# Performance work log

Measured on AMD Instinct MI355X. Metric: run time of the kernel, lower is better.

The kernel has to match this reference:

```python
import jax, jax.numpy as jnp
import numpy as np

N_NODES = 100000
N_EDGES = 1600000
NODE_DIM = 128
HIDDEN_DIM = 128


def _sage_conv(x, src, dst, deg_inv, W_l, W_r, b):
    # PyG SAGEConv (aggr='mean', root_weight=True):
    #   out = lin_l(mean_{j in N(i)} x_j) + lin_r(x_i)
    msgs = x[src]                                             # [E, d_in] gather
    agg = jax.ops.segment_sum(msgs, dst, num_segments=N_NODES)  # [N, d_in]
    mean = agg * deg_inv[:, None]
    return mean @ W_l + x @ W_r + b


def setup_inputs() -> dict:
    key = jax.random.key(0)
    ks = jax.random.split(key, 9)
    x = jax.random.normal(ks[0], (N_NODES, NODE_DIM), dtype=jnp.float32)
    edge_index = jax.random.randint(ks[1], (2, N_EDGES), 0, N_NODES, dtype=jnp.int32)
    t = jnp.zeros((1,), dtype=jnp.float32)

    def glorot(k, fan_in, fan_out):
        s = (6.0 / (fan_in + fan_out)) ** 0.5
        return jax.random.uniform(k, (fan_in, fan_out), jnp.float32, -s, s)

    return {
        "t": t,
        "x": x,
        "edge_index": edge_index,
        "W1_l": glorot(ks[2], NODE_DIM, HIDDEN_DIM),
        "W1_r": glorot(ks[3], NODE_DIM, HIDDEN_DIM),
        "b1": jnp.zeros((HIDDEN_DIM,), jnp.float32),
        "W2_l": glorot(ks[4], HIDDEN_DIM, HIDDEN_DIM),
        "W2_r": glorot(ks[5], HIDDEN_DIM, HIDDEN_DIM),
        "b2": jnp.zeros((HIDDEN_DIM,), jnp.float32),
        "W3_l": glorot(ks[6], HIDDEN_DIM, NODE_DIM),
        "W3_r": glorot(ks[7], HIDDEN_DIM, NODE_DIM),
        "b3": jnp.zeros((NODE_DIM,), jnp.float32),
    }


def reference(t, x, edge_index, W1_l, W1_r, b1, W2_l, W2_r, b2, W3_l, W3_r, b3):
    src, dst = edge_index[0], edge_index[1]
    deg = jax.ops.segment_sum(jnp.ones((N_EDGES,), x.dtype), dst, num_segments=N_NODES)
    deg_inv = jnp.where(deg > 0, 1.0 / jnp.maximum(deg, 1.0), 0.0)

    h = jax.nn.relu(_sage_conv(x, src, dst, deg_inv, W1_l, W1_r, b1))
    h = jax.nn.relu(_sage_conv(h, src, dst, deg_inv, W2_l, W2_r, b2))
    dx_dt = _sage_conv(h, src, dst, deg_inv, W3_l, W3_r, b3)
    return dx_dt
```

## Files before the change

### kernel.cpp

```cpp
#include <hip/hip_runtime.h>

#define NN   100000
#define NE   1600000
#define DIM  128
#define NBKT 391
#define EPB  16384
#define NBLK 98
#define NTILES (NN / 16)
#define CASTB 12500
#define CWB   384

#define NSLC 8
#define GCH  512
#define GATB (((NN + GCH - 1) / GCH) * NSLC)

typedef short          s16x8 __attribute__((ext_vector_type(8)));
typedef unsigned short u16x8 __attribute__((ext_vector_type(8)));
typedef float          f32x4 __attribute__((ext_vector_type(4)));

__device__ __forceinline__ unsigned short f2b(float f) {
    unsigned u = __float_as_uint(f);
    unsigned r = ((u >> 16) & 1u) + 0x7FFFu;
    return (unsigned short)((u + r) >> 16);
}
__device__ __forceinline__ float b2f(unsigned short h) {
    return __uint_as_float(((unsigned)h) << 16);
}

__global__ void k_prep(const float* __restrict__ x, unsigned short* __restrict__ xb,
                       const int* __restrict__ dst, int* __restrict__ hist,
                       const float* __restrict__ W1l, const float* __restrict__ W1r,
                       const float* __restrict__ W2l, const float* __restrict__ W2r,
                       const float* __restrict__ W3l, const float* __restrict__ W3r,
                       unsigned short* __restrict__ Wt1, unsigned short* __restrict__ Wt2,
                       unsigned short* __restrict__ Wt3) {
    __shared__ int lh[NBKT];
    int t = threadIdx.x, b = blockIdx.x;
    if (b < NBLK) {
        for (int j = t; j < NBKT; j += 256) lh[j] = 0;
        __syncthreads();
        int base = b * EPB;
        int end = base + EPB; if (end > NE) end = NE;
        for (int i = base + t; i < end; i += 256) atomicAdd(&lh[dst[i] >> 8], 1);
        __syncthreads();
        for (int j = t; j < NBKT; j += 256) hist[j * NBLK + b] = lh[j];
    } else if (b < NBLK + CASTB) {
        int i = (b - NBLK) * 256 + t;
        int slice = i / (NN * 4);
        int rem = i - slice * (NN * 4);
        int node = rem >> 2;
        int off4 = i & 3;
        float4 v = ((const float4*)x)[node * 32 + slice * 4 + off4];
        ushort4 o;
        o.x = f2b(v.x); o.y = f2b(v.y); o.z = f2b(v.z); o.w = f2b(v.w);
        ((ushort4*)xb)[i] = o;
    } else {
        int i = (b - NBLK - CASTB) * 256 + t;
        int L = i >> 15;
        int rem = i & 32767;
        int n = rem >> 8;
        int k = rem & 255;
        const float* Wl = (L == 0) ? W1l : (L == 1) ? W2l : W3l;
        const float* Wr = (L == 0) ? W1r : (L == 1) ? W2r : W3r;
        unsigned short* Wt = (L == 0) ? Wt1 : (L == 1) ? Wt2 : Wt3;
        float v = (k < 128) ? Wl[k * 128 + n] : Wr[(k - 128) * 128 + n];
        Wt[n * 256 + k] = f2b(v);
    }
}

__global__ void k_scanrow(int* __restrict__ hist, int* __restrict__ row_total) {
    __shared__ int sh[128];
    int k = blockIdx.x, t = threadIdx.x;
    int v = (t < NBLK) ? hist[k * NBLK + t] : 0;
    sh[t] = v;
    __syncthreads();
    for (int off = 1; off < 128; off <<= 1) {
        int a = (t >= off) ? sh[t - off] : 0;
        __syncthreads();
        sh[t] += a;
        __syncthreads();
    }
    if (t < NBLK) hist[k * NBLK + t] = sh[t] - v;
    if (t == 127) row_total[k] = sh[127];
}

__global__ void k_scanbkt(const int* __restrict__ row_total, int* __restrict__ bbase) {
    __shared__ int sh[512];
    int t = threadIdx.x;
    int v = (t < NBKT) ? row_total[t] : 0;
    sh[t] = v;
    __syncthreads();
    for (int off = 1; off < 512; off <<= 1) {
        int a = (t >= off) ? sh[t - off] : 0;
        __syncthreads();
        sh[t] += a;
        __syncthreads();
    }
    if (t < NBKT) bbase[t] = sh[t] - v;
    if (t == NBKT) bbase[NBKT] = NE;
}

__global__ void k_bin2(const int* __restrict__ src, const int* __restrict__ dst,
                       const int* __restrict__ hist, const int* __restrict__ bbase,
                       int* __restrict__ binned) {
    __shared__ int s_base[NBKT];
    __shared__ int s_cnt[NBKT];
    int t = threadIdx.x, b = blockIdx.x;
    for (int j = t; j < NBKT; j += 256) {
        s_base[j] = bbase[j] + hist[j * NBLK + b];
        s_cnt[j] = 0;
    }
    __syncthreads();
    int base = b * EPB;
    int end = base + EPB; if (end > NE) end = NE;
    for (int i = base + t; i < end; i += 256) {
        int d = dst[i];
        int k = d >> 8;
        int w = (src[i] << 8) | (d & 255);
        int lpos = atomicAdd(&s_cnt[k], 1);
        binned[s_base[k] + lpos] = w;
    }
}

__global__ void k_build(const int* __restrict__ binned,
                        const int* __restrict__ bucket_base,
                        int* __restrict__ csr,
                        int* __restrict__ row_start,
                        float* __restrict__ deg_inv) {
    __shared__ int s_deg[256], s_scan[256], s_cur[256];
    __shared__ int stage[8192];
    int b = blockIdx.x, t = threadIdx.x;
    int base = bucket_base[b], end = bucket_base[b + 1];
    int cnt = end - base;
    s_deg[t] = 0;
    __syncthreads();
    for (int i = t; i < cnt; i += 256)
        atomicAdd(&s_deg[binned[base + i] & 255], 1);
    __syncthreads();
    s_scan[t] = s_deg[t];
    __syncthreads();
    for (int off = 1; off < 256; off <<= 1) {
        int a = (t >= off) ? s_scan[t - off] : 0;
        __syncthreads();
        s_scan[t] += a;
        __syncthreads();
    }
    int excl = s_scan[t] - s_deg[t];
    s_cur[t] = excl;
    int node = b * 256 + t;
    if (node < NN) {
        int d = s_deg[t];
        row_start[node] = base + excl;
        deg_inv[node]   = (d > 0) ? 1.0f / (float)d : 0.0f;
    }
    if (b == 0 && t == 0) row_start[NN] = NE;
    __syncthreads();
    for (int i = t; i < cnt; i += 256) {
        int w = binned[base + i];
        int pos = atomicAdd(&s_cur[w & 255], 1);
        int s = w >> 8;
        if (pos < 8192) stage[pos] = s;
        else            csr[base + pos] = s;
    }
    __syncthreads();
    int m = cnt < 8192 ? cnt : 8192;
    for (int i = t; i < m; i += 256) csr[base + i] = stage[i];
}

__global__ void k_gather(const unsigned short* __restrict__ feat,
                         const int* __restrict__ row_start,
                         const float* __restrict__ deg_inv, const int* __restrict__ csr,
                         unsigned short* __restrict__ mean) {
    int b = blockIdx.x;
    int slice = b & (NSLC - 1);
    int chunk = b >> 3;
    int n0 = chunk * GCH;
    int n1 = n0 + GCH; if (n1 > NN) n1 = NN;
    int lane = threadIdx.x & 63;
    int wv   = threadIdx.x >> 6;
    int nsub = lane >> 3;
    int q    = (lane >> 1) & 3;
    int c    = lane & 1;
    const u16x8* fp = ((const u16x8*)feat) + (size_t)slice * (NN * 2);
    u16x8*       mp = ((u16x8*)mean)  + (size_t)slice * (NN * 2);
    for (int bn = n0 + wv * 8; bn < n1; bn += 32) {
        int n = bn + nsub;
        if (n >= n1) continue;
        int rs = row_start[n];
        int re = row_start[n + 1];
        int d = re - rs;
        float acc0[8], acc1[8];
#pragma unroll
        for (int t = 0; t < 8; t++) { acc0[t] = 0.0f; acc1[t] = 0.0f; }
        int j = q;
        for (; j + 4 < d; j += 8) {
            int s0 = csr[rs + j];
            int s1 = csr[rs + j + 4];
            u16x8 v0 = fp[s0 * 2 + c];
            u16x8 v1 = fp[s1 * 2 + c];
#pragma unroll
            for (int t = 0; t < 8; t++) { acc0[t] += b2f(v0[t]); acc1[t] += b2f(v1[t]); }
        }
        if (j < d) {
            int s0 = csr[rs + j];
            u16x8 v0 = fp[s0 * 2 + c];
#pragma unroll
            for (int t = 0; t < 8; t++) acc0[t] += b2f(v0[t]);
        }
#pragma unroll
        for (int t = 0; t < 8; t++) acc0[t] += acc1[t];
#pragma unroll
        for (int t = 0; t < 8; t++) {
            acc0[t] += __shfl_xor(acc0[t], 2, 64);
            acc0[t] += __shfl_xor(acc0[t], 4, 64);
        }
        if (q == 0) {
            float s = deg_inv[n];
            u16x8 o;
#pragma unroll
            for (int t = 0; t < 8; t++) o[t] = f2b(acc0[t] * s);
            mp[n * 2 + c] = o;
        }
    }
}

template <int MODE>
__global__ void __launch_bounds__(512)
k_lin(const unsigned short* __restrict__ meanb,
      const unsigned short* __restrict__ hb,
      const unsigned short* __restrict__ Wt,
      const float* __restrict__ bias, void* __restrict__ out) {
    __shared__ s16x8 sW[4096];
    int t = threadIdx.x;
    const s16x8* wp = (const s16x8*)Wt;
#pragma unroll
    for (int it = 0; it < 8; it++) {
        int ci = it * 512 + t;
        int frag = ci >> 6, ln = ci & 63;
        int mt = frag >> 3, kt = frag & 7;
        int m = mt * 16 + (ln & 15);
        int kc = kt * 4 + (ln >> 4);
        sW[ci] = wp[m * 32 + kc];
    }
    __syncthreads();

    int lane = t & 63;
    int wv   = t >> 6;
    int tile = blockIdx.x * 8 + wv;
    if (tile >= NTILES) return;
    int n0 = tile * 16;
    int q = lane >> 4, c = lane & 15;
    const s16x8* mp = (const s16x8*)meanb;
    const s16x8* hp = (const s16x8*)hb;
    int row = n0 + c;
    s16x8 B[8];
#pragma unroll
    for (int kt = 0; kt < 4; kt++) {
        int kc = kt * 4 + q;
        B[kt] = mp[((kc >> 1) * NN + row) * 2 + (kc & 1)];
    }
#pragma unroll
    for (int kt = 0; kt < 4; kt++) {
        int kc = kt * 4 + q;
        B[4 + kt] = hp[((kc >> 1) * NN + row) * 2 + (kc & 1)];
    }
    const f32x4* bp = (const f32x4*)bias;
#pragma unroll
    for (int mt = 0; mt < 8; mt++) {
        f32x4 acc = {0.f, 0.f, 0.f, 0.f};
#pragma unroll
        for (int kt = 0; kt < 8; kt++)
            acc = __builtin_amdgcn_mfma_f32_16x16x32_bf16(sW[(mt * 8 + kt) * 64 + lane],
                                                          B[kt], acc, 0, 0, 0);
        f32x4 bv = bp[mt * 4 + q];
        int node = n0 + c;
        if (MODE == 0) {
            ushort4 o;
            float v0 = acc[0] + bv[0]; if (v0 < 0.f) v0 = 0.f;
            float v1 = acc[1] + bv[1]; if (v1 < 0.f) v1 = 0.f;
            float v2 = acc[2] + bv[2]; if (v2 < 0.f) v2 = 0.f;
            float v3 = acc[3] + bv[3]; if (v3 < 0.f) v3 = 0.f;
            o.x = f2b(v0); o.y = f2b(v1); o.z = f2b(v2); o.w = f2b(v3);
            ((ushort4*)out)[(mt * NN + node) * 4 + q] = o;
        } else {
            f32x4 v;
#pragma unroll
            for (int r = 0; r < 4; r++) v[r] = acc[r] + bv[r];
            ((f32x4*)out)[node * 32 + mt * 4 + q] = v;
        }
    }
}

extern "C" void kernel_launch(void* const* d_in, const int* in_sizes, int n_in,
                              void* d_out, int out_size, void* d_ws, size_t ws_size,
                              hipStream_t stream) {
    const float* x   = (const float*)d_in[1];
    const int*   ei  = (const int*)d_in[2];
    const int*   src = ei;
    const int*   dst = ei + NE;
    const float* W1l = (const float*)d_in[3];
    const float* W1r = (const float*)d_in[4];
    const float* b1  = (const float*)d_in[5];
    const float* W2l = (const float*)d_in[6];
    const float* W2r = (const float*)d_in[7];
    const float* b2  = (const float*)d_in[8];
    const float* W3l = (const float*)d_in[9];
    const float* W3r = (const float*)d_in[10];
    const float* b3  = (const float*)d_in[11];

    char* w = (char*)d_ws;
    auto carve = [&](size_t bytes) {
        void* p = (void*)w;
        w += (bytes + 255) & ~(size_t)255;
        return p;
    };
    int*   row_start = (int*)carve((NN + 1) * 4);
    float* deg_inv   = (float*)carve(NN * 4);
    int*   hist      = (int*)carve((size_t)NBKT * NBLK * 4);
    int*   row_total = (int*)carve(NBKT * 4);
    int*   bbase     = (int*)carve((NBKT + 1) * 4);
    int*   csr       = (int*)carve((size_t)NE * 4);
    unsigned short* Wt1 = (unsigned short*)carve(128 * 256 * 2);
    unsigned short* Wt2 = (unsigned short*)carve(128 * 256 * 2);
    unsigned short* Wt3 = (unsigned short*)carve(128 * 256 * 2);
    unsigned short* xb    = (unsigned short*)carve((size_t)NN * DIM * 2);
    unsigned short* meanb = (unsigned short*)carve((size_t)NN * DIM * 2);
    unsigned short* h1b   = (unsigned short*)carve((size_t)NN * DIM * 2);
    unsigned short* h2b   = xb;
    int*   binned    = (int*)meanb;

    k_prep<<<NBLK + CASTB + CWB, 256, 0, stream>>>(x, xb, dst, hist,
                                                   W1l, W1r, W2l, W2r, W3l, W3r,
                                                   Wt1, Wt2, Wt3);
    k_scanrow<<<NBKT, 128, 0, stream>>>(hist, row_total);
    k_scanbkt<<<1, 512, 0, stream>>>(row_total, bbase);
    k_bin2<<<NBLK, 256, 0, stream>>>(src, dst, hist, bbase, binned);
    k_build<<<NBKT, 256, 0, stream>>>(binned, bbase, csr, row_start, deg_inv);

    const int LB = (NTILES + 7) / 8;

    k_gather<<<GATB, 256, 0, stream>>>(xb, row_start, deg_inv, csr, meanb);
    k_lin<0><<<LB, 512, 0, stream>>>(meanb, xb, Wt1, b1, (void*)h1b);
    k_gather<<<GATB, 256, 0, stream>>>(h1b, row_start, deg_inv, csr, meanb);
    k_lin<0><<<LB, 512, 0, stream>>>(meanb, h1b, Wt2, b2, (void*)h2b);
    k_gather<<<GATB, 256, 0, stream>>>(h2b, row_start, deg_inv, csr, meanb);
    k_lin<1><<<LB, 512, 0, stream>>>(meanb, h2b, Wt3, b3, d_out);
}
```

Measured before the change: 511.3 us.

## Sort nodes by degree into packed metadata to balance gather waves

Builds a per-degree histogram during CSR construction, scans it, and permutes nodes into degree-sorted order. Each node gets a packed int4 record holding row start, degree, inverse degree and node id. The gather kernel walks this sorted list, so the nodes sharing a wavefront have similar neighbor counts, which cuts loop divergence and tail imbalance. The chunk size per block is also halved. The cost is two extra small kernels, global atomics, and output rows written in scattered rather than contiguous node order.

```diff
diff --git a/kernel.cpp b/kernel.cpp
--- a/kernel.cpp
+++ b/kernel.cpp
@@ -11,8 +11,9 @@
 #define CWB   384
 
 #define NSLC 8
-#define GCH  512
-#define GATB (((NN + GCH - 1) / GCH) * NSLC)
+#define GCH  256
+#define NCHK ((NN + GCH - 1) / GCH)
+#define GATB (NCHK * NSLC)
 
 typedef short          s16x8 __attribute__((ext_vector_type(8)));
 typedef unsigned short u16x8 __attribute__((ext_vector_type(8)));
@@ -84,9 +85,11 @@
     if (t == 127) row_total[k] = sh[127];
 }
 
-__global__ void k_scanbkt(const int* __restrict__ row_total, int* __restrict__ bbase) {
+__global__ void k_scanbkt(const int* __restrict__ row_total, int* __restrict__ bbase,
+                          int* __restrict__ dcnt) {
     __shared__ int sh[512];
     int t = threadIdx.x;
+    if (t < 64) dcnt[t] = 0;
     int v = (t < NBKT) ? row_total[t] : 0;
     sh[t] = v;
     __syncthreads();
@@ -126,13 +129,15 @@
                         const int* __restrict__ bucket_base,
                         int* __restrict__ csr,
                         int* __restrict__ row_start,
-                        float* __restrict__ deg_inv) {
+                        int* __restrict__ dcnt) {
     __shared__ int s_deg[256], s_scan[256], s_cur[256];
+    __shared__ int dh[64];
     __shared__ int stage[8192];
     int b = blockIdx.x, t = threadIdx.x;
     int base = bucket_base[b], end = bucket_base[b + 1];
     int cnt = end - base;
     s_deg[t] = 0;
+    if (t < 64) dh[t] = 0;
     __syncthreads();
     for (int i = t; i < cnt; i += 256)
         atomicAdd(&s_deg[binned[base + i] & 255], 1);
@@ -151,7 +156,7 @@
     if (node < NN) {
         int d = s_deg[t];
         row_start[node] = base + excl;
-        deg_inv[node]   = (d > 0) ? 1.0f / (float)d : 0.0f;
+        atomicAdd(&dh[d < 63 ? d : 63], 1);
     }
     if (b == 0 && t == 0) row_start[NN] = NE;
     __syncthreads();
@@ -165,11 +170,40 @@
     __syncthreads();
     int m = cnt < 8192 ? cnt : 8192;
     for (int i = t; i < m; i += 256) csr[base + i] = stage[i];
+    if (t < 64) { int v = dh[t]; if (v) atomicAdd(&dcnt[t], v); }
+}
+
+__global__ void k_dscan(const int* __restrict__ dcnt, int* __restrict__ dbase) {
+    __shared__ int sh[64];
+    int t = threadIdx.x;
+    int v = dcnt[t];
+    sh[t] = v;
+    __syncthreads();
+    for (int off = 1; off < 64; off <<= 1) {
+        int a = (t >= off) ? sh[t - off] : 0;
+        __syncthreads();
+        sh[t] += a;
+        __syncthreads();
+    }
+    dbase[t] = sh[t] - v;
+}
+
+__global__ void k_perm(const int* __restrict__ row_start, int* __restrict__ dbase,
+                       int4* __restrict__ meta) {
+    int n = blockIdx.x * 256 + threadIdx.x;
+    if (n >= NN) return;
+    int rs = row_start[n];
+    int d  = row_start[n + 1] - rs;
+    int dc = d < 63 ? d : 63;
+    int slot = atomicAdd(&dbase[dc], 1);
+    float di = (d > 0) ? 1.0f / (float)d : 0.0f;
+    int4 M; M.x = rs; M.y = d; M.z = __float_as_int(di); M.w = n;
+    meta[slot] = M;
 }
 
 __global__ void k_gather(const unsigned short* __restrict__ feat,
-                         const int* __restrict__ row_start,
-                         const float* __restrict__ deg_inv, const int* __restrict__ csr,
+                         const int4* __restrict__ meta,
+                         const int* __restrict__ csr,
                          unsigned short* __restrict__ mean) {
     int b = blockIdx.x;
     int slice = b & (NSLC - 1);
@@ -184,11 +218,10 @@
     const u16x8* fp = ((const u16x8*)feat) + (size_t)slice * (NN * 2);
     u16x8*       mp = ((u16x8*)mean)  + (size_t)slice * (NN * 2);
     for (int bn = n0 + wv * 8; bn < n1; bn += 32) {
-        int n = bn + nsub;
-        if (n >= n1) continue;
-        int rs = row_start[n];
-        int re = row_start[n + 1];
-        int d = re - rs;
+        int4 M = meta[bn + nsub];
+        int rs = M.x, d = M.y;
+        float dinv = __int_as_float(M.z);
+        int n = M.w;
         float acc0[8], acc1[8];
 #pragma unroll
         for (int t = 0; t < 8; t++) { acc0[t] = 0.0f; acc1[t] = 0.0f; }
@@ -215,10 +248,9 @@
             acc0[t] += __shfl_xor(acc0[t], 4, 64);
         }
         if (q == 0) {
-            float s = deg_inv[n];
             u16x8 o;
 #pragma unroll
-            for (int t = 0; t < 8; t++) o[t] = f2b(acc0[t] * s);
+            for (int t = 0; t < 8; t++) o[t] = f2b(acc0[t] * dinv);
             mp[n * 2 + c] = o;
         }
     }
@@ -315,7 +347,9 @@
         return p;
     };
     int*   row_start = (int*)carve((NN + 1) * 4);
-    float* deg_inv   = (float*)carve(NN * 4);
+    int*   dcnt      = (int*)carve(64 * 4);
+    int*   dbase     = (int*)carve(64 * 4);
+    int4*  meta      = (int4*)carve((size_t)NN * 16);
     int*   hist      = (int*)carve((size_t)NBKT * NBLK * 4);
     int*   row_total = (int*)carve(NBKT * 4);
     int*   bbase     = (int*)carve((NBKT + 1) * 4);
@@ -333,16 +367,18 @@
                                                    W1l, W1r, W2l, W2r, W3l, W3r,
                                                    Wt1, Wt2, Wt3);
     k_scanrow<<<NBKT, 128, 0, stream>>>(hist, row_total);
-    k_scanbkt<<<1, 512, 0, stream>>>(row_total, bbase);
+    k_scanbkt<<<1, 512, 0, stream>>>(row_total, bbase, dcnt);
     k_bin2<<<NBLK, 256, 0, stream>>>(src, dst, hist, bbase, binned);
-    k_build<<<NBKT, 256, 0, stream>>>(binned, bbase, csr, row_start, deg_inv);
+    k_build<<<NBKT, 256, 0, stream>>>(binned, bbase, csr, row_start, dcnt);
+    k_dscan<<<1, 64, 0, stream>>>(dcnt, dbase);
+    k_perm<<<NBKT, 256, 0, stream>>>(row_start, dbase, meta);
 
     const int LB = (NTILES + 7) / 8;
 
-    k_gather<<<GATB, 256, 0, stream>>>(xb, row_start, deg_inv, csr, meanb);
+    k_gather<<<GATB, 256, 0, stream>>>(xb, meta, csr, meanb);
     k_lin<0><<<LB, 512, 0, stream>>>(meanb, xb, Wt1, b1, (void*)h1b);
-    k_gather<<<GATB, 256, 0, stream>>>(h1b, row_start, deg_inv, csr, meanb);
+    k_gather<<<GATB, 256, 0, stream>>>(h1b, meta, csr, meanb);
     k_lin<0><<<LB, 512, 0, stream>>>(meanb, h1b, Wt2, b2, (void*)h2b);
-    k_gather<<<GATB, 256, 0, stream>>>(h2b, row_start, deg_inv, csr, meanb);
+    k_gather<<<GATB, 256, 0, stream>>>(h2b, meta, csr, meanb);
     k_lin<1><<<LB, 512, 0, stream>>>(meanb, h2b, Wt3, b3, d_out);
 }
```

Result: slower. 830.6 us (+62.5%).
